# Performance work log

Measured on AMD Instinct MI355X. Metric: run time of the kernel, lower is better.

## Reference

```python
import jax, jax.numpy as jnp
import numpy as np

B, S, H = 4, 4096, 2048


def setup_inputs() -> dict:
    key = jax.random.key(0)
    ks = jax.random.split(key, 20)
    def lin(k, fin, fout):
        # torch nn.Linear default init: U(-1/sqrt(fin), 1/sqrt(fin))
        kw, kb = jax.random.split(k)
        bound = 1.0 / np.sqrt(fin)
        W = jax.random.uniform(kw, (fin, fout), jnp.float32, -bound, bound)
        b = jax.random.uniform(kb, (fout,), jnp.float32, -bound, bound)
        return W, b
    hidden_states = jax.random.normal(ks[0], (B, S, H), jnp.float32)
    access_frequency = jax.random.uniform(ks[1], (B, S), jnp.float32)
    importance_score = jax.random.uniform(ks[2], (B, S), jnp.float32)
    sel_W1, sel_b1 = lin(ks[3], H, H // 4)
    sel_W2, sel_b2 = lin(ks[4], H // 4, 3)
    c1_W, c1_b = lin(ks[5], H, H // 2)
    f1_W, f1_b = lin(ks[6], H // 2, H // 2)
    d1_W, d1_b = lin(ks[7], H // 2, H)
    c2_W, c2_b = lin(ks[8], H, H // 4)
    f2_W, f2_b = lin(ks[9], H // 4, H // 4)
    d2_W, d2_b = lin(ks[10], H // 4, H)
    return dict(hidden_states=hidden_states, access_frequency=access_frequency,
                importance_score=importance_score, sel_W1=sel_W1, sel_b1=sel_b1,
                sel_W2=sel_W2, sel_b2=sel_b2, c1_W=c1_W, c1_b=c1_b, f1_W=f1_W,
                f1_b=f1_b, d1_W=d1_W, d1_b=d1_b, c2_W=c2_W, c2_b=c2_b,
                f2_W=f2_W, f2_b=f2_b, d2_W=d2_W, d2_b=d2_b)


def reference(hidden_states, access_frequency, importance_score,
              sel_W1, sel_b1, sel_W2, sel_b2,
              c1_W, c1_b, f1_W, f1_b, d1_W, d1_b,
              c2_W, c2_b, f2_W, f2_b, d2_W, d2_b):
    x = hidden_states  # [B,S,H]
    Hh = x.shape[-1] // 2
    # strategy selector on frequency/importance-modulated features
    combined = jnp.concatenate(
        [x[..., :Hh] * access_frequency[..., None],
         x[..., Hh:] * importance_score[..., None]], axis=-1)  # [B,S,H]
    hmid = jax.nn.relu(jnp.einsum('bsh,hk->bsk', combined, sel_W1) + sel_b1)
    weights = jax.nn.softmax(jnp.einsum('bsk,kl->bsl', hmid, sel_W2) + sel_b2)
    sel = jnp.argmax(weights, axis=-1)  # [B,S] in {0,1,2}
    # expert paths (computed densely, selected per token)
    out1 = (jax.numpy.einsum('bsh,hc->bsc', x, c1_W) + c1_b)
    out1 = jnp.einsum('bsc,cd->bsd', out1, f1_W) + f1_b
    out1 = jnp.einsum('bsc,ch->bsh', out1, d1_W) + d1_b
    out2 = (jnp.einsum('bsh,hc->bsc', x, c2_W) + c2_b)
    out2 = jnp.einsum('bsc,cd->bsd', out2, f2_W) + f2_b
    out2 = jnp.einsum('bsc,ch->bsh', out2, d2_W) + d2_b
    s = sel[..., None]
    out = jnp.where(s == 0, x, jnp.where(s == 1, out1, out2))
    return out
```

## Files before the change

kernel.cpp:

```cpp
#include <hip/hip_runtime.h>


#define RECHECK_TAU 0.008

typedef __bf16 bf16x8 __attribute__((ext_vector_type(8)));
typedef float  f32x4  __attribute__((ext_vector_type(4)));
typedef unsigned short us;

__device__ __forceinline__ float bf2f(us u) {
  union { unsigned u; float f; } v; v.u = ((unsigned)u) << 16;
  return v.f;
}
__device__ __forceinline__ us f2bf(float f) {
  union { float f; unsigned u; } v; v.f = f;
  unsigned r = v.u + 0x7fffu + ((v.u >> 16) & 1u);
  return (us)(r >> 16);
}
__device__ __forceinline__ float scrub(float v) {
  return (v == v && fabsf(v) < 1e30f) ? v : 0.f;
}
__device__ __forceinline__ void gld_lds16(const void* g, void* l) {
  __builtin_amdgcn_global_load_lds(
      (const __attribute__((address_space(1))) void*)g,
      (__attribute__((address_space(3))) void*)l, 16, 0, 0);
}

__global__ __launch_bounds__(256) void xprep(
    const float* __restrict__ X, const float* __restrict__ FR,
    const float* __restrict__ IM, us* __restrict__ Xb, us* __restrict__ Xm)
{
  const int t = blockIdx.x;
  const int j = threadIdx.x;
  const float fr = FR[t], im = IM[t];
  const float md = (j < 128) ? fr : im;
  const float4* src = (const float4*)(X + (size_t)t * 2048);
  float4 a0 = src[2 * j], a1 = src[2 * j + 1];
  float av[8] = {a0.x, a0.y, a0.z, a0.w, a1.x, a1.y, a1.z, a1.w};
  union { uint4 v; us u[8]; } b, m;
#pragma unroll
  for (int k = 0; k < 8; ++k) {
    b.u[k] = f2bf(av[k]);
    m.u[k] = f2bf(av[k] * md);
  }
  ((uint4*)(Xb + (size_t)t * 2048))[j] = b.v;
  ((uint4*)(Xm + (size_t)t * 2048))[j] = m.v;
}

template<int MODE, int AIDX>
__global__ __launch_bounds__(256) void gemm_bt(
    const us* __restrict__ Ap, const us* __restrict__ BT,
    const float* __restrict__ bias, void* __restrict__ outp,
    const int* __restrict__ aidx, const int* __restrict__ oidx,
    const int* __restrict__ cntp, int N, int K)
{
  const int cnt = cntp ? cntp[0] : (int)(gridDim.x << 7);
  const int Mp  = (cnt + 127) & ~127;
  const int bm0 = blockIdx.x * 128;
  if (bm0 >= Mp) return;
  const int bn0 = blockIdx.y * 128;

  __shared__ __align__(16) us As[128 * 64];
  __shared__ __align__(16) us Bs[128 * 64];
  const int tid  = threadIdx.x;
  const int lane = tid & 63;
  const int w    = tid >> 6;
  const int wr   = w >> 1, wc = w & 1;

  const us* gb[4];
  const us* ga[4];
  us* la[4]; us* lb[4];
#pragma unroll
  for (int i = 0; i < 4; ++i) {
    const int s = i * 256 + tid, m = s >> 3, cp = s & 7, c = cp ^ (m & 7);
    gb[i] = BT + (size_t)(bn0 + m) * K + c * 8;
    lb[i] = &Bs[s * 8];
    la[i] = &As[s * 8];
    const int arow = AIDX ? aidx[bm0 + m] : (bm0 + m);
    ga[i] = Ap + (size_t)arow * K + c * 8;
  }

  f32x4 acc[4][4] = {};

  for (int k0 = 0; k0 < K; k0 += 64) {
#pragma unroll
    for (int i = 0; i < 4; ++i) { gld_lds16(gb[i], lb[i]); gb[i] += 64; }
#pragma unroll
    for (int i = 0; i < 4; ++i) { gld_lds16(ga[i], la[i]); ga[i] += 64; }
    __syncthreads();
#pragma unroll
    for (int kk = 0; kk < 2; ++kk) {
      const int cc = kk * 4 + (lane >> 4);
      bf16x8 af[4], bfr[4];
#pragma unroll
      for (int t = 0; t < 4; ++t) {
        const int m = wr * 64 + t * 16 + (lane & 15);
        const int n = wc * 64 + t * 16 + (lane & 15);
        af[t]  = *(const bf16x8*)&As[(m * 8 + (cc ^ (m & 7))) * 8];
        bfr[t] = *(const bf16x8*)&Bs[(n * 8 + (cc ^ (n & 7))) * 8];
      }
#pragma unroll
      for (int mt = 0; mt < 4; ++mt)
#pragma unroll
        for (int nt = 0; nt < 4; ++nt)
          acc[mt][nt] = __builtin_amdgcn_mfma_f32_16x16x32_bf16(
              af[mt], bfr[nt], acc[mt][nt], 0, 0, 0);
    }
    __syncthreads();
  }

  const int colb = bn0 + wc * 64 + (lane & 15);
  const int rowb = bm0 + wr * 64 + ((lane >> 4) << 2);
  float bv[4];
#pragma unroll
  for (int nt = 0; nt < 4; ++nt) bv[nt] = bias[colb + nt * 16];
#pragma unroll
  for (int mt = 0; mt < 4; ++mt) {
#pragma unroll
    for (int r = 0; r < 4; ++r) {
      const int row = rowb + mt * 16 + r;
      if (MODE == 3) {
        if (row >= cnt) continue;
        const size_t orow = (size_t)oidx[row];
#pragma unroll
        for (int nt = 0; nt < 4; ++nt)
          ((float*)outp)[orow * N + colb + nt * 16] =
              scrub(acc[mt][nt][r] + bv[nt]);
      } else if (MODE == 4) {
#pragma unroll
        for (int nt = 0; nt < 4; ++nt)
          ((float*)outp)[(size_t)row * N + colb + nt * 16] =
              fmaxf(scrub(acc[mt][nt][r] + bv[nt]), 0.f);
      } else {
#pragma unroll
        for (int nt = 0; nt < 4; ++nt)
          ((us*)outp)[(size_t)row * N + colb + nt * 16] =
              f2bf(scrub(acc[mt][nt][r] + bv[nt]));
      }
    }
  }
}

__global__ __launch_bounds__(256) void logits_gap(
    const float* __restrict__ hmid, const float* __restrict__ W2,
    const float* __restrict__ B2, int* __restrict__ sel,
    int* __restrict__ cntr, int* __restrict__ ridx)
{
  const int lane = threadIdx.x & 63;
  const int wv   = threadIdx.x >> 6;
  const int t    = blockIdx.x * 4 + wv;
  const float* h = hmid + (size_t)t * 512;
  double s0 = 0.0, s1 = 0.0, s2 = 0.0;
#pragma unroll
  for (int j = 0; j < 8; ++j) {
    int e = j * 64 + lane;
    double hv = (double)h[e];
    s0 += hv * (double)W2[e * 3 + 0];
    s1 += hv * (double)W2[e * 3 + 1];
    s2 += hv * (double)W2[e * 3 + 2];
  }
  for (int o = 32; o > 0; o >>= 1) {
    s0 += __shfl_down(s0, o);
    s1 += __shfl_down(s1, o);
    s2 += __shfl_down(s2, o);
  }
  if (lane == 0) {
    s0 += (double)B2[0]; s1 += (double)B2[1]; s2 += (double)B2[2];
    int idx = 0; double b = s0;
    if (s1 > b) { b = s1; idx = 1; }
    if (s2 > b) { b = s2; idx = 2; }
    sel[t] = idx;
    const double mn = fmin(fmin(s0, s1), s2);
    const double second = (s0 + s1 + s2) - b - mn;
    if (b - second < RECHECK_TAU) {
      const int p = atomicAdd(cntr, 1);
      ridx[p] = t;
    }
  }
}

__global__ __launch_bounds__(256) void recheck(
    const float* __restrict__ X, const float* __restrict__ FR,
    const float* __restrict__ IM, const float* __restrict__ W1,
    const float* __restrict__ B1, const float* __restrict__ W2,
    const float* __restrict__ B2, const int* __restrict__ cntr,
    const int* __restrict__ ridx, int* __restrict__ sel)
{
  const int nr = cntr[0];
  const int r0 = blockIdx.x * 4;
  if (r0 >= nr) return;

  __shared__ __align__(16) float comb[4][2048];
  __shared__ float red[4][4][3];
  const int tid  = threadIdx.x;
  const int lane = tid & 63;
  const int wv   = tid >> 6;

  int toks[4];
#pragma unroll
  for (int i = 0; i < 4; ++i) {
    const int r    = r0 + i;
    const bool lv  = (r < nr);
    const int tok  = lv ? ridx[r] : ridx[r0];
    toks[i] = lv ? tok : -1;
    const float md = (tid < 128) ? FR[tok] : IM[tok];
    const float4* src = (const float4*)(X + (size_t)tok * 2048);
    float4 a0 = src[2 * tid], a1 = src[2 * tid + 1];
    float* c = &comb[i][8 * tid];
    c[0] = a0.x * md; c[1] = a0.y * md; c[2] = a0.z * md; c[3] = a0.w * md;
    c[4] = a1.x * md; c[5] = a1.y * md; c[6] = a1.z * md; c[7] = a1.w * md;
  }
  __syncthreads();

  float z[4][2] = {};
  const float* wp = W1 + 2 * tid;
  const float4* cb[4] = {(const float4*)comb[0], (const float4*)comb[1],
                         (const float4*)comb[2], (const float4*)comb[3]};
#pragma unroll 4
  for (int k4 = 0; k4 < 512; ++k4) {
    const float4 c0 = cb[0][k4], c1 = cb[1][k4], c2 = cb[2][k4], c3 = cb[3][k4];
    const float* wk = wp + (size_t)k4 * 2048;
    const float2 wA = *(const float2*)(wk);
    const float2 wB = *(const float2*)(wk + 512);
    const float2 wC = *(const float2*)(wk + 1024);
    const float2 wD = *(const float2*)(wk + 1536);
    z[0][0] = fmaf(c0.x, wA.x, z[0][0]); z[0][1] = fmaf(c0.x, wA.y, z[0][1]);
    z[1][0] = fmaf(c1.x, wA.x, z[1][0]); z[1][1] = fmaf(c1.x, wA.y, z[1][1]);
    z[2][0] = fmaf(c2.x, wA.x, z[2][0]); z[2][1] = fmaf(c2.x, wA.y, z[2][1]);
    z[3][0] = fmaf(c3.x, wA.x, z[3][0]); z[3][1] = fmaf(c3.x, wA.y, z[3][1]);
    z[0][0] = fmaf(c0.y, wB.x, z[0][0]); z[0][1] = fmaf(c0.y, wB.y, z[0][1]);
    z[1][0] = fmaf(c1.y, wB.x, z[1][0]); z[1][1] = fmaf(c1.y, wB.y, z[1][1]);
    z[2][0] = fmaf(c2.y, wB.x, z[2][0]); z[2][1] = fmaf(c2.y, wB.y, z[2][1]);
    z[3][0] = fmaf(c3.y, wB.x, z[3][0]); z[3][1] = fmaf(c3.y, wB.y, z[3][1]);
    z[0][0] = fmaf(c0.z, wC.x, z[0][0]); z[0][1] = fmaf(c0.z, wC.y, z[0][1]);
    z[1][0] = fmaf(c1.z, wC.x, z[1][0]); z[1][1] = fmaf(c1.z, wC.y, z[1][1]);
    z[2][0] = fmaf(c2.z, wC.x, z[2][0]); z[2][1] = fmaf(c2.z, wC.y, z[2][1]);
    z[3][0] = fmaf(c3.z, wC.x, z[3][0]); z[3][1] = fmaf(c3.z, wC.y, z[3][1]);
    z[0][0] = fmaf(c0.w, wD.x, z[0][0]); z[0][1] = fmaf(c0.w, wD.y, z[0][1]);
    z[1][0] = fmaf(c1.w, wD.x, z[1][0]); z[1][1] = fmaf(c1.w, wD.y, z[1][1]);
    z[2][0] = fmaf(c2.w, wD.x, z[2][0]); z[2][1] = fmaf(c2.w, wD.y, z[2][1]);
    z[3][0] = fmaf(c3.w, wD.x, z[3][0]); z[3][1] = fmaf(c3.w, wD.y, z[3][1]);
  }

  const float b0 = B1[2 * tid], b1 = B1[2 * tid + 1];
  const float w20 = W2[(2 * tid) * 3 + 0], w21 = W2[(2 * tid) * 3 + 1],
              w22 = W2[(2 * tid) * 3 + 2];
  const float w30 = W2[(2 * tid + 1) * 3 + 0], w31 = W2[(2 * tid + 1) * 3 + 1],
              w32 = W2[(2 * tid + 1) * 3 + 2];
#pragma unroll
  for (int i = 0; i < 4; ++i) {
    const float h0 = fmaxf(z[i][0] + b0, 0.f);
    const float h1 = fmaxf(z[i][1] + b1, 0.f);
    float p0 = h0 * w20 + h1 * w30;
    float p1 = h0 * w21 + h1 * w31;
    float p2 = h0 * w22 + h1 * w32;
    for (int o = 32; o > 0; o >>= 1) {
      p0 += __shfl_down(p0, o);
      p1 += __shfl_down(p1, o);
      p2 += __shfl_down(p2, o);
    }
    if (lane == 0) { red[wv][i][0] = p0; red[wv][i][1] = p1; red[wv][i][2] = p2; }
  }
  __syncthreads();
  if (tid < 4) {
    const int i = tid;
    if (toks[i] >= 0) {
      const float s0 = red[0][i][0] + red[1][i][0] + red[2][i][0] + red[3][i][0] + B2[0];
      const float s1 = red[0][i][1] + red[1][i][1] + red[2][i][1] + red[3][i][1] + B2[1];
      const float s2 = red[0][i][2] + red[1][i][2] + red[2][i][2] + red[3][i][2] + B2[2];
      int idx = 0; float b = s0;
      if (s1 > b) { b = s1; idx = 1; }
      if (s2 > b) { idx = 2; }
      sel[toks[i]] = idx;
    }
  }
}

__global__ __launch_bounds__(256) void compact(
    const int* __restrict__ sel, int* __restrict__ cnt,
    int* __restrict__ idx1, int* __restrict__ idx2)
{
  const int t    = blockIdx.x * 256 + threadIdx.x;
  const int lane = threadIdx.x & 63;
  const int w    = threadIdx.x >> 6;
  const int s    = sel[t];
  const bool f1 = (s == 1), f2 = (s == 2);
  const unsigned long long m1 = __ballot(f1);
  const unsigned long long m2 = __ballot(f2);
  const unsigned long long lt = (1ull << lane) - 1ull;
  const int b1 = __popcll(m1 & lt);
  const int b2 = __popcll(m2 & lt);
  __shared__ int w1[4], w2[4], base1, base2;
  if (lane == 0) { w1[w] = __popcll(m1); w2[w] = __popcll(m2); }
  __syncthreads();
  if (threadIdx.x == 0) {
    base1 = atomicAdd(&cnt[0], w1[0] + w1[1] + w1[2] + w1[3]);
    base2 = atomicAdd(&cnt[1], w2[0] + w2[1] + w2[2] + w2[3]);
  }
  __syncthreads();
  int o1 = base1, o2 = base2;
  for (int i = 0; i < w; ++i) { o1 += w1[i]; o2 += w2[i]; }
  if (f1) idx1[o1 + b1] = t;
  if (f2) idx2[o2 + b2] = t;
}

__global__ __launch_bounds__(128) void pad_idx(
    const int* __restrict__ cnt, int* __restrict__ idx1, int* __restrict__ idx2)
{
  idx1[cnt[0] + threadIdx.x] = 0;
  idx2[cnt[1] + threadIdx.x] = 0;
}

__global__ __launch_bounds__(256) void pass0(
    const float* __restrict__ X, const int* __restrict__ sel,
    float* __restrict__ OUT)
{
  const int t = blockIdx.x;
  if (sel[t] != 0) return;
  const uint4* src = (const uint4*)(X + (size_t)t * 2048);
  uint4* dst = (uint4*)(OUT + (size_t)t * 2048);
  dst[threadIdx.x]       = src[threadIdx.x];
  dst[threadIdx.x + 256] = src[threadIdx.x + 256];
}

__global__ __launch_bounds__(256) void transpose_f2b(
    const float* __restrict__ W, us* __restrict__ WT, int K, int N)
{
  __shared__ float tile[32][33];
  const int tx = threadIdx.x & 31, ty = threadIdx.x >> 5;
  const int n0 = blockIdx.x * 32, k0 = blockIdx.y * 32;
#pragma unroll
  for (int r = 0; r < 4; ++r)
    tile[ty + r * 8][tx] = W[(size_t)(k0 + ty + r * 8) * N + n0 + tx];
  __syncthreads();
#pragma unroll
  for (int r = 0; r < 4; ++r)
    WT[(size_t)(n0 + ty + r * 8) * K + k0 + tx] = f2bf(tile[tx][ty + r * 8]);
}

extern "C" void kernel_launch(void* const* d_in, const int* in_sizes, int n_in,
                              void* d_out, int out_size, void* d_ws, size_t ws_size,
                              hipStream_t stream) {
  const float* X   = (const float*)d_in[0];
  const float* FR  = (const float*)d_in[1];
  const float* IM  = (const float*)d_in[2];
  const float* W1  = (const float*)d_in[3];
  const float* B1  = (const float*)d_in[4];
  const float* W2  = (const float*)d_in[5];
  const float* B2  = (const float*)d_in[6];
  const float* C1W = (const float*)d_in[7];
  const float* C1B = (const float*)d_in[8];
  const float* F1W = (const float*)d_in[9];
  const float* F1B = (const float*)d_in[10];
  const float* D1W = (const float*)d_in[11];
  const float* D1B = (const float*)d_in[12];
  const float* C2W = (const float*)d_in[13];
  const float* C2B = (const float*)d_in[14];
  const float* F2W = (const float*)d_in[15];
  const float* F2B = (const float*)d_in[16];
  const float* D2W = (const float*)d_in[17];
  const float* D2B = (const float*)d_in[18];
  float* OUT = (float*)d_out;

  size_t off = 0;
  auto alloc = [&](size_t bytes) -> void* {
    void* p = (char*)d_ws + off;
    off += (bytes + 255) & ~(size_t)255;
    return p;
  };
  us* WT_selH = (us*)alloc(512ull * 2048 * 2);
  us* WT_c1   = (us*)alloc(1024ull * 2048 * 2);
  us* WT_f1   = (us*)alloc(1024ull * 1024 * 2);
  us* WT_d1   = (us*)alloc(2048ull * 1024 * 2);
  us* WT_c2   = (us*)alloc(512ull * 2048 * 2);
  us* WT_f2   = (us*)alloc(512ull * 512 * 2);
  us* WT_d2   = (us*)alloc(2048ull * 512 * 2);
  int* sel    = (int*)alloc(16384ull * 4);
  int* cnt    = (int*)alloc(3 * 4);
  int* idx1   = (int*)alloc((16384ull + 128) * 4);
  int* idx2   = (int*)alloc((16384ull + 128) * 4);
  int* ridx   = (int*)alloc(16384ull * 4);
  us*  Xb     = (us*)alloc(16384ull * 2048 * 2);
  void* R1    = alloc(16384ull * 1024 * 2);
  void* R2    = alloc(16384ull * 2048 * 2);
  if (ws_size < off) return;

  us*    Xm   = (us*)R2;
  float* hmid = (float*)R1;
  us* t1 = (us*)R1;
  us* u1 = (us*)R1;
  us* t2 = (us*)R2;
  us* u2 = (us*)R2;

  const dim3 blk(256);
  transpose_f2b<<<dim3(16, 64), blk, 0, stream>>>(W1, WT_selH, 2048, 512);
  transpose_f2b<<<dim3(32, 64), blk, 0, stream>>>(C1W, WT_c1, 2048, 1024);
  transpose_f2b<<<dim3(32, 32), blk, 0, stream>>>(F1W, WT_f1, 1024, 1024);
  transpose_f2b<<<dim3(64, 32), blk, 0, stream>>>(D1W, WT_d1, 1024, 2048);
  transpose_f2b<<<dim3(16, 64), blk, 0, stream>>>(C2W, WT_c2, 2048, 512);
  transpose_f2b<<<dim3(16, 16), blk, 0, stream>>>(F2W, WT_f2, 512, 512);
  transpose_f2b<<<dim3(64, 16), blk, 0, stream>>>(D2W, WT_d2, 512, 2048);

  hipMemsetAsync(cnt, 0, 12, stream);

  xprep<<<dim3(16384), blk, 0, stream>>>(X, FR, IM, Xb, Xm);

  gemm_bt<4, 0><<<dim3(128, 4), blk, 0, stream>>>(
      Xm, WT_selH, B1, hmid, nullptr, nullptr, nullptr, 512, 2048);
  logits_gap<<<dim3(4096), blk, 0, stream>>>(hmid, W2, B2, sel, cnt + 2, ridx);

  recheck<<<dim3(4096), blk, 0, stream>>>(X, FR, IM, W1, B1, W2, B2,
                                          cnt + 2, ridx, sel);

  compact<<<dim3(64), blk, 0, stream>>>(sel, cnt, idx1, idx2);
  pad_idx<<<dim3(1), dim3(128), 0, stream>>>(cnt, idx1, idx2);

  pass0<<<dim3(16384), blk, 0, stream>>>(X, sel, OUT);

  gemm_bt<0, 1><<<dim3(128, 8), blk, 0, stream>>>(Xb, WT_c1, C1B, t1, idx1, nullptr, cnt + 0, 1024, 2048);
  gemm_bt<0, 0><<<dim3(128, 8), blk, 0, stream>>>(t1, WT_f1, F1B, t2, nullptr, nullptr, cnt + 0, 1024, 1024);
  gemm_bt<3, 0><<<dim3(128, 16), blk, 0, stream>>>(t2, WT_d1, D1B, OUT, nullptr, idx1, cnt + 0, 2048, 1024);

  gemm_bt<0, 1><<<dim3(128, 4), blk, 0, stream>>>(Xb, WT_c2, C2B, u1, idx2, nullptr, cnt + 1, 512, 2048);
  gemm_bt<0, 0><<<dim3(128, 4), blk, 0, stream>>>(u1, WT_f2, F2B, u2, nullptr, nullptr, cnt + 1, 512, 512);
  gemm_bt<3, 0><<<dim3(128, 16), blk, 0, stream>>>(u2, WT_d2, D2B, OUT, nullptr, idx2, cnt + 1, 2048, 512);
}
```

Measured before the change: 738.2 us.

## Split fp32 recheck GEMV across output-column blocks with a separate finalize kernel

The fp32 recheck of near-tie tokens now splits the 512 hidden columns across four blocks in gridDim.y. Each thread computes 4 columns over a K slice, with a shared-memory reduction over 8 K partitions. Each block writes partial logits to a new plog buffer, and a small recheck_fin kernel sums the partials and writes the selection. This is meant to raise parallelism and coalesce W1 loads as float4 when few tokens are rechecked. The cost is an extra kernel launch, extra shared memory and a global round-trip for the partials.

```diff
diff --git a/kernel.cpp b/kernel.cpp
--- a/kernel.cpp
+++ b/kernel.cpp
@@ -178,101 +178,129 @@
   }
 }
 
-__global__ __launch_bounds__(256) void recheck(
+__global__ __launch_bounds__(256) void recheck_part(
     const float* __restrict__ X, const float* __restrict__ FR,
     const float* __restrict__ IM, const float* __restrict__ W1,
     const float* __restrict__ B1, const float* __restrict__ W2,
-    const float* __restrict__ B2, const int* __restrict__ cntr,
-    const int* __restrict__ ridx, int* __restrict__ sel)
+    const int* __restrict__ cntr, const int* __restrict__ ridx,
+    float* __restrict__ plog)
 {
   const int nr = cntr[0];
   const int r0 = blockIdx.x * 4;
   if (r0 >= nr) return;
+  const int n0 = blockIdx.y * 128;
 
   __shared__ __align__(16) float comb[4][2048];
-  __shared__ float red[4][4][3];
-  const int tid  = threadIdx.x;
-  const int lane = tid & 63;
-  const int wv   = tid >> 6;
-
-  int toks[4];
-#pragma unroll
-  for (int i = 0; i < 4; ++i) {
-    const int r    = r0 + i;
-    const bool lv  = (r < nr);
-    const int tok  = lv ? ridx[r] : ridx[r0];
-    toks[i] = lv ? tok : -1;
-    const float md = (tid < 128) ? FR[tok] : IM[tok];
-    const float4* src = (const float4*)(X + (size_t)tok * 2048);
-    float4 a0 = src[2 * tid], a1 = src[2 * tid + 1];
-    float* c = &comb[i][8 * tid];
-    c[0] = a0.x * md; c[1] = a0.y * md; c[2] = a0.z * md; c[3] = a0.w * md;
-    c[4] = a1.x * md; c[5] = a1.y * md; c[6] = a1.z * md; c[7] = a1.w * md;
+  __shared__ float red[8][4][128];
+
+  const int tid = threadIdx.x;
+  const int kp  = tid >> 5;
+  const int cg  = tid & 31;
+
+  int toks[4]; float frv[4], imv[4];
+#pragma unroll
+  for (int t = 0; t < 4; ++t) {
+    const int r  = r0 + t;
+    const int tk = (r < nr) ? ridx[r] : ridx[r0];
+    toks[t] = tk;
+    frv[t] = FR[tk];
+    imv[t] = IM[tk];
+  }
+#pragma unroll
+  for (int j = 0; j < 8; ++j) {
+    const int g = tid + 256 * j;
+    const int t = g >> 9, e = g & 511;
+    const float md = (e < 256) ? frv[t] : imv[t];
+    float4 v = *(const float4*)(X + (size_t)toks[t] * 2048 + 4 * e);
+    v.x *= md; v.y *= md; v.z *= md; v.w *= md;
+    *(float4*)&comb[t][4 * e] = v;
   }
   __syncthreads();
 
-  float z[4][2] = {};
-  const float* wp = W1 + 2 * tid;
-  const float4* cb[4] = {(const float4*)comb[0], (const float4*)comb[1],
-                         (const float4*)comb[2], (const float4*)comb[3]};
-#pragma unroll 4
-  for (int k4 = 0; k4 < 512; ++k4) {
-    const float4 c0 = cb[0][k4], c1 = cb[1][k4], c2 = cb[2][k4], c3 = cb[3][k4];
-    const float* wk = wp + (size_t)k4 * 2048;
-    const float2 wA = *(const float2*)(wk);
-    const float2 wB = *(const float2*)(wk + 512);
-    const float2 wC = *(const float2*)(wk + 1024);
-    const float2 wD = *(const float2*)(wk + 1536);
-    z[0][0] = fmaf(c0.x, wA.x, z[0][0]); z[0][1] = fmaf(c0.x, wA.y, z[0][1]);
-    z[1][0] = fmaf(c1.x, wA.x, z[1][0]); z[1][1] = fmaf(c1.x, wA.y, z[1][1]);
-    z[2][0] = fmaf(c2.x, wA.x, z[2][0]); z[2][1] = fmaf(c2.x, wA.y, z[2][1]);
-    z[3][0] = fmaf(c3.x, wA.x, z[3][0]); z[3][1] = fmaf(c3.x, wA.y, z[3][1]);
-    z[0][0] = fmaf(c0.y, wB.x, z[0][0]); z[0][1] = fmaf(c0.y, wB.y, z[0][1]);
-    z[1][0] = fmaf(c1.y, wB.x, z[1][0]); z[1][1] = fmaf(c1.y, wB.y, z[1][1]);
-    z[2][0] = fmaf(c2.y, wB.x, z[2][0]); z[2][1] = fmaf(c2.y, wB.y, z[2][1]);
-    z[3][0] = fmaf(c3.y, wB.x, z[3][0]); z[3][1] = fmaf(c3.y, wB.y, z[3][1]);
-    z[0][0] = fmaf(c0.z, wC.x, z[0][0]); z[0][1] = fmaf(c0.z, wC.y, z[0][1]);
-    z[1][0] = fmaf(c1.z, wC.x, z[1][0]); z[1][1] = fmaf(c1.z, wC.y, z[1][1]);
-    z[2][0] = fmaf(c2.z, wC.x, z[2][0]); z[2][1] = fmaf(c2.z, wC.y, z[2][1]);
-    z[3][0] = fmaf(c3.z, wC.x, z[3][0]); z[3][1] = fmaf(c3.z, wC.y, z[3][1]);
-    z[0][0] = fmaf(c0.w, wD.x, z[0][0]); z[0][1] = fmaf(c0.w, wD.y, z[0][1]);
-    z[1][0] = fmaf(c1.w, wD.x, z[1][0]); z[1][1] = fmaf(c1.w, wD.y, z[1][1]);
-    z[2][0] = fmaf(c2.w, wD.x, z[2][0]); z[2][1] = fmaf(c2.w, wD.y, z[2][1]);
-    z[3][0] = fmaf(c3.w, wD.x, z[3][0]); z[3][1] = fmaf(c3.w, wD.y, z[3][1]);
-  }
-
-  const float b0 = B1[2 * tid], b1 = B1[2 * tid + 1];
-  const float w20 = W2[(2 * tid) * 3 + 0], w21 = W2[(2 * tid) * 3 + 1],
-              w22 = W2[(2 * tid) * 3 + 2];
-  const float w30 = W2[(2 * tid + 1) * 3 + 0], w31 = W2[(2 * tid + 1) * 3 + 1],
-              w32 = W2[(2 * tid + 1) * 3 + 2];
-#pragma unroll
-  for (int i = 0; i < 4; ++i) {
-    const float h0 = fmaxf(z[i][0] + b0, 0.f);
-    const float h1 = fmaxf(z[i][1] + b1, 0.f);
-    float p0 = h0 * w20 + h1 * w30;
-    float p1 = h0 * w21 + h1 * w31;
-    float p2 = h0 * w22 + h1 * w32;
-    for (int o = 32; o > 0; o >>= 1) {
-      p0 += __shfl_down(p0, o);
-      p1 += __shfl_down(p1, o);
-      p2 += __shfl_down(p2, o);
+  float z[4][4] = {};
+  const float* wbase = W1 + n0 + cg * 4;
+#pragma unroll 2
+  for (int k4 = 0; k4 < 64; ++k4) {
+    const int kb = kp * 256 + 4 * k4;
+    const float4 w0 = *(const float4*)(wbase + (size_t)(kb + 0) * 512);
+    const float4 w1 = *(const float4*)(wbase + (size_t)(kb + 1) * 512);
+    const float4 w2 = *(const float4*)(wbase + (size_t)(kb + 2) * 512);
+    const float4 w3 = *(const float4*)(wbase + (size_t)(kb + 3) * 512);
+#pragma unroll
+    for (int t = 0; t < 4; ++t) {
+      const float4 c = *(const float4*)&comb[t][kb];
+      z[t][0] = fmaf(c.x, w0.x, z[t][0]);
+      z[t][1] = fmaf(c.x, w0.y, z[t][1]);
+      z[t][2] = fmaf(c.x, w0.z, z[t][2]);
+      z[t][3] = fmaf(c.x, w0.w, z[t][3]);
+      z[t][0] = fmaf(c.y, w1.x, z[t][0]);
+      z[t][1] = fmaf(c.y, w1.y, z[t][1]);
+      z[t][2] = fmaf(c.y, w1.z, z[t][2]);
+      z[t][3] = fmaf(c.y, w1.w, z[t][3]);
+      z[t][0] = fmaf(c.z, w2.x, z[t][0]);
+      z[t][1] = fmaf(c.z, w2.y, z[t][1]);
+      z[t][2] = fmaf(c.z, w2.z, z[t][2]);
+      z[t][3] = fmaf(c.z, w2.w, z[t][3]);
+      z[t][0] = fmaf(c.w, w3.x, z[t][0]);
+      z[t][1] = fmaf(c.w, w3.y, z[t][1]);
+      z[t][2] = fmaf(c.w, w3.z, z[t][2]);
+      z[t][3] = fmaf(c.w, w3.w, z[t][3]);
     }
-    if (lane == 0) { red[wv][i][0] = p0; red[wv][i][1] = p1; red[wv][i][2] = p2; }
+  }
+
+#pragma unroll
+  for (int t = 0; t < 4; ++t) {
+    red[kp][t][cg * 4 + 0] = z[t][0];
+    red[kp][t][cg * 4 + 1] = z[t][1];
+    red[kp][t][cg * 4 + 2] = z[t][2];
+    red[kp][t][cg * 4 + 3] = z[t][3];
   }
   __syncthreads();
-  if (tid < 4) {
-    const int i = tid;
-    if (toks[i] >= 0) {
-      const float s0 = red[0][i][0] + red[1][i][0] + red[2][i][0] + red[3][i][0] + B2[0];
-      const float s1 = red[0][i][1] + red[1][i][1] + red[2][i][1] + red[3][i][1] + B2[1];
-      const float s2 = red[0][i][2] + red[1][i][2] + red[2][i][2] + red[3][i][2] + B2[2];
-      int idx = 0; float b = s0;
-      if (s1 > b) { b = s1; idx = 1; }
-      if (s2 > b) { idx = 2; }
-      sel[toks[i]] = idx;
+
+  if (tid < 32) {
+#pragma unroll
+    for (int t = 0; t < 4; ++t) {
+      float p0 = 0.f, p1 = 0.f, p2 = 0.f;
+#pragma unroll
+      for (int j = 0; j < 4; ++j) {
+        const int ci = tid * 4 + j;
+        float zf = 0.f;
+#pragma unroll
+        for (int q = 0; q < 8; ++q) zf += red[q][t][ci];
+        const int n = n0 + ci;
+        const float h = fmaxf(zf + B1[n], 0.f);
+        p0 = fmaf(h, W2[n * 3 + 0], p0);
+        p1 = fmaf(h, W2[n * 3 + 1], p1);
+        p2 = fmaf(h, W2[n * 3 + 2], p2);
+      }
+      for (int o = 16; o > 0; o >>= 1) {
+        p0 += __shfl_down(p0, o, 32);
+        p1 += __shfl_down(p1, o, 32);
+        p2 += __shfl_down(p2, o, 32);
+      }
+      if (tid == 0 && (r0 + t) < nr) {
+        float* d = plog + (size_t)(r0 + t) * 12 + blockIdx.y * 3;
+        d[0] = p0; d[1] = p1; d[2] = p2;
+      }
     }
   }
+}
+
+__global__ __launch_bounds__(256) void recheck_fin(
+    const float* __restrict__ plog, const float* __restrict__ B2,
+    const int* __restrict__ cntr, const int* __restrict__ ridx,
+    int* __restrict__ sel)
+{
+  const int r = blockIdx.x * 256 + threadIdx.x;
+  if (r >= cntr[0]) return;
+  const float* p = plog + (size_t)r * 12;
+  const float s0 = p[0] + p[3] + p[6] + p[9]  + B2[0];
+  const float s1 = p[1] + p[4] + p[7] + p[10] + B2[1];
+  const float s2 = p[2] + p[5] + p[8] + p[11] + B2[2];
+  int idx = 0; float b = s0;
+  if (s1 > b) { b = s1; idx = 1; }
+  if (s2 > b) { idx = 2; }
+  sel[ridx[r]] = idx;
 }
 
 __global__ __launch_bounds__(256) void compact(
@@ -379,6 +407,7 @@
   int* idx1   = (int*)alloc((16384ull + 128) * 4);
   int* idx2   = (int*)alloc((16384ull + 128) * 4);
   int* ridx   = (int*)alloc(16384ull * 4);
+  float* plog = (float*)alloc(16384ull * 12 * 4);
   us*  Xb     = (us*)alloc(16384ull * 2048 * 2);
   void* R1    = alloc(16384ull * 1024 * 2);
   void* R2    = alloc(16384ull * 2048 * 2);
@@ -408,8 +437,9 @@
       Xm, WT_selH, B1, hmid, nullptr, nullptr, nullptr, 512, 2048);
   logits_gap<<<dim3(4096), blk, 0, stream>>>(hmid, W2, B2, sel, cnt + 2, ridx);
 
-  recheck<<<dim3(4096), blk, 0, stream>>>(X, FR, IM, W1, B1, W2, B2,
-                                          cnt + 2, ridx, sel);
+  recheck_part<<<dim3(4096, 4), blk, 0, stream>>>(X, FR, IM, W1, B1, W2,
+                                                  cnt + 2, ridx, plog);
+  recheck_fin<<<dim3(64), blk, 0, stream>>>(plog, B2, cnt + 2, ridx, sel);
 
   compact<<<dim3(64), blk, 0, stream>>>(sel, cnt, idx1, idx2);
   pad_idx<<<dim3(1), dim3(128), 0, stream>>>(cnt, idx1, idx2);
```

After: 691.1 us. 1.07x faster.
